# Kernel optimization log

Hardware: AMD Instinct MI355X
Metric: run time of the kernel (lower is better)

The kernel has to match this reference:

```python
import jax, jax.numpy as jnp
import numpy as np

B, N, D, OUT = 4, 4096, 2048, 2048
E, RANK, TOP_K = 8, 16, 2
ALPHA = 16.0
SCALING = ALPHA / RANK


def setup_inputs() -> dict:
    key = jax.random.key(0)
    k1, k2, k3, k4 = jax.random.split(key, 4)
    x = jax.random.normal(k1, (B, N, D), dtype=jnp.float32)
    weight = jax.random.normal(k2, (OUT, D), dtype=jnp.float32) * (1.0 / np.sqrt(D))
    router_w = jax.random.normal(k3, (E, D), dtype=jnp.float32) * 0.02
    experts_A = jax.random.normal(k4, (E, D, RANK), dtype=jnp.float32) * (1.0 / np.sqrt(RANK))
    # experts_B is zero-initialized in the module; use small random values so the
    # LoRA branch contributes non-trivially to the output for kernel testing.
    experts_B = jax.random.normal(jax.random.fold_in(key, 5), (E, RANK, OUT), dtype=jnp.float32) * 0.02
    return {"x": x, "weight": weight, "router_w": router_w,
            "experts_A": experts_A, "experts_B": experts_B}


def reference(x, weight, router_w, experts_A, experts_B):
    # base = F.linear(x, weight)  (no bias)
    base = jnp.einsum('bnd,od->bno', x, weight)
    # router logits: x @ W_r^T -> (B, N, E)
    logits = jnp.einsum('bnd,ed->bne', x, router_w)
    # top-k sparse routing: keep top-k logits, set rest to -inf, softmax
    topk_vals, topk_idx = jax.lax.top_k(logits, TOP_K)  # (B,N,K)
    keep = jax.nn.one_hot(topk_idx, E, dtype=jnp.bool_).any(axis=-2)  # (B,N,E)
    masked = jnp.where(keep, logits, -jnp.inf)
    router_weights = jax.nn.softmax(masked, axis=-1)  # (B,N,E)
    # per-expert low-rank down/up projection, weighted by router
    lora_down = jnp.einsum('bnd,edr->bner', x, experts_A)  # (B,N,E,rank)
    weighted = lora_down * router_weights[..., None]
    moe_out = jnp.einsum('bner,erd->bnd', weighted, experts_B)  # (B,N,OUT)
    return base + SCALING * moe_out
```

## Files before the change

kernel.cpp:

```cpp
#include <hip/hip_runtime.h>
#include <stdint.h>

#define D_DIM 2048
#define OUT_DIM 2048
#define NTOK 16384
#define SCALING 1.0f
#define NT32 68

typedef unsigned short u16;
typedef __attribute__((ext_vector_type(8))) short s16x8;
typedef __attribute__((ext_vector_type(4))) float f32x4;

#define WZ_OFF  0u
#define AZ_OFF  8388608u
#define BZ_OFF  8912896u
#define CZ_OFF  9437184u
#define W8_OFF  13631488u
#define XB_OFF  14155776u
#define WS_BIG   81264640u

__device__ inline u16 f2bf(float f) {
  union { float f; uint32_t u; } v; v.f = f;
  uint32_t u = v.u;
  u += 0x7FFFu + ((u >> 16) & 1u);
  return (u16)(u >> 16);
}

__device__ inline int swz32(int c, int row) {
  return (c & ~31) | (((((c >> 3) & 3) ^ ((row >> 1) & 3))) << 3) | (c & 7);
}

__global__ __launch_bounds__(256) void k_prep_router(
    const float* __restrict__ W, const float* __restrict__ A,
    const float* __restrict__ Bf, const float* __restrict__ x,
    const float* __restrict__ rw,
    u16* __restrict__ Wz, u16* __restrict__ Az, u16* __restrict__ Bz,
    float* __restrict__ w8, u16* __restrict__ xb) {
  int bid = blockIdx.x;
  if (bid < 4096) {
    int idx = bid * 256 + threadIdx.x;
    int o  = idx >> 9;
    int k0 = (idx & 511) * 4;
    const float4 v = *(const float4*)&W[(size_t)o * D_DIM + k0];
    int dst = swz32(k0, o);
    uint32_t p0 = (uint32_t)f2bf(v.x) | ((uint32_t)f2bf(v.y) << 16);
    uint32_t p1 = (uint32_t)f2bf(v.z) | ((uint32_t)f2bf(v.w) << 16);
    *(uint2*)&Wz[(size_t)o * D_DIM + dst] = make_uint2(p0, p1);
    return;
  }
  if (bid < 5120) {
    int idx = (bid - 4096) * 256 + threadIdx.x;
    float v = A[idx];
    int r = idx & 15;
    int d = (idx >> 4) & 2047;
    int e = idx >> 15;
    int er = e * 16 + r;
    Az[(size_t)er * D_DIM + swz32(d, er)] = f2bf(v);
    return;
  }
  if (bid < 6144) {
    int idx = (bid - 5120) * 256 + threadIdx.x;
    float v = Bf[idx];
    int er = idx >> 11;
    int o  = idx & 2047;
    Bz[(size_t)o * 128 + swz32(er, o)] = f2bf(v);
    return;
  }
  int lane = threadIdx.x & 63, wid = threadIdx.x >> 6;
  int t = (bid - 6144) * 4 + wid;
  const float* xr = x + (size_t)t * D_DIM;
  float4 xv[8];
#pragma unroll
  for (int j = 0; j < 8; ++j) xv[j] = *(const float4*)&xr[j * 256 + lane * 4];
#pragma unroll
  for (int j = 0; j < 8; ++j) {
    int c4 = j * 256 + lane * 4;
    int dst = swz32(c4, t);
    uint32_t p0 = (uint32_t)f2bf(xv[j].x) | ((uint32_t)f2bf(xv[j].y) << 16);
    uint32_t p1 = (uint32_t)f2bf(xv[j].z) | ((uint32_t)f2bf(xv[j].w) << 16);
    *(uint2*)&xb[(size_t)t * D_DIM + dst] = make_uint2(p0, p1);
  }
  float lg[8];
#pragma unroll
  for (int e = 0; e < 8; ++e) {
    float a = 0.f;
#pragma unroll
    for (int j = 0; j < 8; ++j) {
      float4 rv = *(const float4*)&rw[e * D_DIM + j * 256 + lane * 4];
      a = fmaf(xv[j].x, rv.x, a); a = fmaf(xv[j].y, rv.y, a);
      a = fmaf(xv[j].z, rv.z, a); a = fmaf(xv[j].w, rv.w, a);
    }
#pragma unroll
    for (int off = 32; off; off >>= 1) a += __shfl_xor(a, off, 64);
    lg[e] = a;
  }
  int i0 = 0;
#pragma unroll
  for (int e = 1; e < 8; ++e) if (lg[e] > lg[i0]) i0 = e;
  int i1 = (i0 == 0) ? 1 : 0;
#pragma unroll
  for (int e = 0; e < 8; ++e) if (e != i0 && lg[e] > lg[i1]) i1 = e;
  float e1 = expf(lg[i1] - lg[i0]);
  float inv = 1.f / (1.f + e1);
  float w0 = inv * SCALING, w1 = e1 * inv * SCALING;
  if (lane < 8)
    w8[(size_t)t * 8 + lane] = (lane == i0) ? w0 : (lane == i1) ? w1 : 0.f;
}

__global__ __launch_bounds__(256) void k_lora64(const u16* __restrict__ xb,
                                                const u16* __restrict__ Az,
                                                const float* __restrict__ w8,
                                                u16* __restrict__ Cz) {
  __shared__ u16 Al[2][2][64 * 32];
  __shared__ u16 Bl[2][2][128 * 32];
  __shared__ float w8s[64 * 8];
  int tid = threadIdx.x, lane = tid & 63, wid = tid >> 6;
  int t0 = blockIdx.x * 64;
  w8s[tid] = w8[(size_t)t0 * 8 + tid];
  w8s[256 + tid] = w8[(size_t)t0 * 8 + 256 + tid];
  f32x4 acc[8];
#pragma unroll
  for (int n = 0; n < 8; ++n) acc[n] = (f32x4){0.f, 0.f, 0.f, 0.f};
  const int l15 = lane & 15;
  const int gA = (lane >> 4) ^ ((l15 >> 1) & 3);
  const int arow = tid >> 2, c8 = (tid & 3) * 8;

  auto stage = [&](int kc, int buf) {
    if (kc > 31) kc = 31;
#pragma unroll
    for (int kk = 0; kk < 2; ++kk) {
      const u16* ga = xb + (size_t)(t0 + arow) * D_DIM + kc * 64 + kk * 32 + c8;
      __builtin_amdgcn_global_load_lds(
          (const __attribute__((address_space(1))) void*)ga,
          (__attribute__((address_space(3))) void*)(&Al[buf][kk][0] + tid * 8), 16, 0, 0);
#pragma unroll
      for (int i = 0; i < 2; ++i) {
        const u16* gb = Az + (size_t)(i * 64 + arow) * D_DIM + kc * 64 + kk * 32 + c8;
        __builtin_amdgcn_global_load_lds(
            (const __attribute__((address_space(1))) void*)gb,
            (__attribute__((address_space(3))) void*)(&Bl[buf][kk][0] + i * 2048 + tid * 8), 16, 0, 0);
      }
    }
  };

  stage(0, 0);
  asm volatile("s_waitcnt vmcnt(0)" ::: "memory");
  __builtin_amdgcn_s_barrier();
  const int aoff = (wid * 16 + l15) * 32 + gA * 8;
  for (int kc = 0; kc < 32; ++kc) {
    int cur = kc & 1;
    stage(kc + 1, cur ^ 1);
#pragma unroll
    for (int kk = 0; kk < 2; ++kk) {
      s16x8 af = *(const s16x8*)&Al[cur][kk][aoff];
#pragma unroll
      for (int nf = 0; nf < 8; ++nf) {
        s16x8 bf = *(const s16x8*)&Bl[cur][kk][(nf * 16 + l15) * 32 + gA * 8];
        acc[nf] = __builtin_amdgcn_mfma_f32_16x16x32_bf16(af, bf, acc[nf], 0, 0, 0);
      }
    }
    asm volatile("s_waitcnt vmcnt(0)" ::: "memory");
    __builtin_amdgcn_s_barrier();
  }
#pragma unroll
  for (int q = 0; q < 4; ++q) {
    int rloc = wid * 16 + (lane >> 4) * 4 + q;
#pragma unroll
    for (int nf = 0; nf < 8; ++nf) {
      int er = nf * 16 + l15;
      float v = acc[nf][q] * w8s[rloc * 8 + (er >> 4)];
      Cz[(size_t)(t0 + rloc) * 128 + swz32(er, rloc)] = f2bf(v);
    }
  }
}

__global__ __launch_bounds__(512, 2) void k_main32(const u16* __restrict__ xb,
                                                   const u16* __restrict__ Wz,
                                                   const u16* __restrict__ Cz,
                                                   const u16* __restrict__ Bz,
                                                   float* __restrict__ out) {
  __shared__ u16 AL[4][8192];
  __shared__ u16 BL[4][8192];
  const int tid = threadIdx.x, lane = tid & 63;
  const int wid = tid >> 6, wm = wid >> 2, wn = wid & 3;
  int bid = blockIdx.x;
  int swz = (bid & 7) * 64 + (bid >> 3);
  int mt = swz >> 3, nt = swz & 7;
  int t0 = mt * 256, o0 = nt * 256;
  const int l15 = lane & 15;
  const int gA = (lane >> 4) ^ ((l15 >> 1) & 3);
  const int aoff = (wm * 128 + l15) * 32 + gA * 8;
  const int boff = (wn * 64 + l15) * 32 + gA * 8;
  const int srow = tid >> 2, sc8 = (tid & 3) * 8;

  f32x4 acc[8][4];
#pragma unroll
  for (int m = 0; m < 8; ++m)
#pragma unroll
    for (int n = 0; n < 4; ++n) acc[m][n] = (f32x4){0.f, 0.f, 0.f, 0.f};
  s16x8 aA[8], bA[4], aB[8], bB[4];

  auto stg = [&](int t, int bufi) {
    if (t > NT32 - 1) t = NT32 - 1;
    const u16 *sa, *sb; int lda, ldb, ca;
    if (t < 64) { sa = xb; lda = D_DIM; sb = Wz; ldb = D_DIM; ca = t * 32; }
    else        { sa = Cz; lda = 128;   sb = Bz; ldb = 128;   ca = (t - 64) * 32; }
#pragma unroll
    for (int i = 0; i < 2; ++i) {
      const u16* g = sa + (size_t)(t0 + i * 128 + srow) * lda + ca + sc8;
      __builtin_amdgcn_global_load_lds(
          (const __attribute__((address_space(1))) void*)g,
          (__attribute__((address_space(3))) void*)(&AL[bufi][0] + i * 4096 + tid * 8), 16, 0, 0);
    }
#pragma unroll
    for (int i = 0; i < 2; ++i) {
      const u16* g = sb + (size_t)(o0 + i * 128 + srow) * ldb + ca + sc8;
      __builtin_amdgcn_global_load_lds(
          (const __attribute__((address_space(1))) void*)g,
          (__attribute__((address_space(3))) void*)(&BL[bufi][0] + i * 4096 + tid * 8), 16, 0, 0);
    }
  };

#define RD(av, bv, bufi) do {                                           \
    const u16* ap_ = &AL[bufi][aoff];                                   \
    const u16* bp_ = &BL[bufi][boff];                                   \
    _Pragma("unroll") for (int i_ = 0; i_ < 8; ++i_)                    \
      av[i_] = *(const s16x8*)(ap_ + i_ * 512);                         \
    _Pragma("unroll") for (int j_ = 0; j_ < 4; ++j_)                    \
      bv[j_] = *(const s16x8*)(bp_ + j_ * 512);                         \
  } while (0)

#define MM(av, bv) do {                                                 \
    _Pragma("unroll") for (int mf_ = 0; mf_ < 8; ++mf_)                 \
      _Pragma("unroll") for (int nf_ = 0; nf_ < 4; ++nf_)               \
        acc[mf_][nf_] = __builtin_amdgcn_mfma_f32_16x16x32_bf16(        \
            av[mf_], bv[nf_], acc[mf_][nf_], 0, 0, 0);                  \
  } while (0)

  stg(0, 0); stg(1, 1); stg(2, 2);
  asm volatile("s_waitcnt vmcnt(4)" ::: "memory");
  __builtin_amdgcn_s_barrier();
  RD(aA, bA, 0);

  for (int jj = 0; jj < NT32; jj += 2) {
    RD(aB, bB, (jj + 1) & 3);
    MM(aA, bA);
    stg(jj + 3, (jj + 3) & 3);
    asm volatile("s_waitcnt vmcnt(4)" ::: "memory");
    __builtin_amdgcn_s_barrier();
    RD(aA, bA, (jj + 2) & 3);
    MM(aB, bB);
    stg(jj + 4, (jj + 4) & 3);
    asm volatile("s_waitcnt vmcnt(4)" ::: "memory");
    __builtin_amdgcn_s_barrier();
  }
  asm volatile("s_waitcnt vmcnt(0) lgkmcnt(0)" ::: "memory");
#undef RD
#undef MM

#pragma unroll
  for (int mf = 0; mf < 8; ++mf)
#pragma unroll
    for (int q = 0; q < 4; ++q) {
      int row = t0 + wm * 128 + mf * 16 + (lane >> 4) * 4 + q;
#pragma unroll
      for (int nf = 0; nf < 4; ++nf) {
        int col = o0 + wn * 64 + nf * 16 + l15;
        out[(size_t)row * OUT_DIM + col] = acc[mf][nf][q];
      }
    }
}

extern "C" void kernel_launch(void* const* d_in, const int* in_sizes, int n_in,
                              void* d_out, int out_size, void* d_ws, size_t ws_size,
                              hipStream_t stream) {
  const float* x  = (const float*)d_in[0];
  const float* W  = (const float*)d_in[1];
  const float* rw = (const float*)d_in[2];
  const float* eA = (const float*)d_in[3];
  const float* eB = (const float*)d_in[4];
  float* out = (float*)d_out;
  char* ws = (char*)d_ws;
  if (ws_size < WS_BIG) return;

  u16*   Wz = (u16*)(ws + WZ_OFF);
  u16*   Az = (u16*)(ws + AZ_OFF);
  u16*   Bz = (u16*)(ws + BZ_OFF);
  u16*   Cz = (u16*)(ws + CZ_OFF);
  float* w8 = (float*)(ws + W8_OFF);
  u16*   xb = (u16*)(ws + XB_OFF);

  k_prep_router<<<10240, 256, 0, stream>>>(W, eA, eB, x, rw, Wz, Az, Bz, w8, xb);
  k_lora64<<<256, 256, 0, stream>>>(xb, Az, w8, Cz);
  k_main32<<<512, 512, 0, stream>>>(xb, Wz, Cz, Bz, out);
}
```

Baseline: 243.9 us.

## Fuse router and x conversion into LoRA kernel; shrink main GEMM tile to 128x128

Moves the x-to-bf16 conversion and router logit/top-2 softmax out of the prep kernel and into the LoRA down-projection kernel. That kernel reads fp32 x directly, writes both xb and its LDS tile, and accumulates router partial sums along the way, which removes the separate w8 buffer and one read of xb. The main GEMM changes from 256x256 tiles with 512 threads and a 4-stage buffer to 128x128 tiles with 256 threads and double buffering. This trades operand reuse for more blocks and occupancy. The fused LoRA kernel now runs only 256 blocks doing scalar conversion work, which could serialise x conversion on few CUs.

Measured after the change: 257.8 us. 1.06x slower.

```diff
diff --git a/kernel.cpp b/kernel.cpp
--- a/kernel.cpp
+++ b/kernel.cpp
@@ -15,7 +15,6 @@
 #define AZ_OFF  8388608u
 #define BZ_OFF  8912896u
 #define CZ_OFF  9437184u
-#define W8_OFF  13631488u
 #define XB_OFF  14155776u
 #define WS_BIG   81264640u
 
@@ -30,12 +29,16 @@
   return (c & ~31) | (((((c >> 3) & 3) ^ ((row >> 1) & 3))) << 3) | (c & 7);
 }
 
-__global__ __launch_bounds__(256) void k_prep_router(
-    const float* __restrict__ W, const float* __restrict__ A,
-    const float* __restrict__ Bf, const float* __restrict__ x,
-    const float* __restrict__ rw,
-    u16* __restrict__ Wz, u16* __restrict__ Az, u16* __restrict__ Bz,
-    float* __restrict__ w8, u16* __restrict__ xb) {
+#define GLDS(gp, lp) __builtin_amdgcn_global_load_lds( \
+    (const __attribute__((address_space(1))) void*)(gp), \
+    (__attribute__((address_space(3))) void*)(lp), 16, 0, 0)
+
+__global__ __launch_bounds__(256) void k_prep(const float* __restrict__ W,
+                                              const float* __restrict__ A,
+                                              const float* __restrict__ Bf,
+                                              u16* __restrict__ Wz,
+                                              u16* __restrict__ Az,
+                                              u16* __restrict__ Bz) {
   int bid = blockIdx.x;
   if (bid < 4096) {
     int idx = bid * 256 + threadIdx.x;
@@ -58,147 +61,155 @@
     Az[(size_t)er * D_DIM + swz32(d, er)] = f2bf(v);
     return;
   }
-  if (bid < 6144) {
+  {
     int idx = (bid - 5120) * 256 + threadIdx.x;
     float v = Bf[idx];
     int er = idx >> 11;
     int o  = idx & 2047;
     Bz[(size_t)o * 128 + swz32(er, o)] = f2bf(v);
-    return;
-  }
-  int lane = threadIdx.x & 63, wid = threadIdx.x >> 6;
-  int t = (bid - 6144) * 4 + wid;
-  const float* xr = x + (size_t)t * D_DIM;
-  float4 xv[8];
-#pragma unroll
-  for (int j = 0; j < 8; ++j) xv[j] = *(const float4*)&xr[j * 256 + lane * 4];
-#pragma unroll
-  for (int j = 0; j < 8; ++j) {
-    int c4 = j * 256 + lane * 4;
-    int dst = swz32(c4, t);
-    uint32_t p0 = (uint32_t)f2bf(xv[j].x) | ((uint32_t)f2bf(xv[j].y) << 16);
-    uint32_t p1 = (uint32_t)f2bf(xv[j].z) | ((uint32_t)f2bf(xv[j].w) << 16);
-    *(uint2*)&xb[(size_t)t * D_DIM + dst] = make_uint2(p0, p1);
-  }
-  float lg[8];
-#pragma unroll
-  for (int e = 0; e < 8; ++e) {
-    float a = 0.f;
-#pragma unroll
-    for (int j = 0; j < 8; ++j) {
-      float4 rv = *(const float4*)&rw[e * D_DIM + j * 256 + lane * 4];
-      a = fmaf(xv[j].x, rv.x, a); a = fmaf(xv[j].y, rv.y, a);
-      a = fmaf(xv[j].z, rv.z, a); a = fmaf(xv[j].w, rv.w, a);
-    }
-#pragma unroll
-    for (int off = 32; off; off >>= 1) a += __shfl_xor(a, off, 64);
-    lg[e] = a;
-  }
-  int i0 = 0;
-#pragma unroll
-  for (int e = 1; e < 8; ++e) if (lg[e] > lg[i0]) i0 = e;
-  int i1 = (i0 == 0) ? 1 : 0;
-#pragma unroll
-  for (int e = 0; e < 8; ++e) if (e != i0 && lg[e] > lg[i1]) i1 = e;
-  float e1 = expf(lg[i1] - lg[i0]);
-  float inv = 1.f / (1.f + e1);
-  float w0 = inv * SCALING, w1 = e1 * inv * SCALING;
-  if (lane < 8)
-    w8[(size_t)t * 8 + lane] = (lane == i0) ? w0 : (lane == i1) ? w1 : 0.f;
-}
-
-__global__ __launch_bounds__(256) void k_lora64(const u16* __restrict__ xb,
-                                                const u16* __restrict__ Az,
-                                                const float* __restrict__ w8,
-                                                u16* __restrict__ Cz) {
-  __shared__ u16 Al[2][2][64 * 32];
-  __shared__ u16 Bl[2][2][128 * 32];
+  }
+}
+
+__global__ __launch_bounds__(256) void k_router_lora(
+    const float* __restrict__ x, const float* __restrict__ rw,
+    const u16* __restrict__ Az, u16* __restrict__ xb, u16* __restrict__ Cz) {
+  __shared__ u16 Axl[2][64 * 64];
+  __shared__ u16 Bzl[2][128 * 64];
   __shared__ float w8s[64 * 8];
   int tid = threadIdx.x, lane = tid & 63, wid = tid >> 6;
   int t0 = blockIdx.x * 64;
-  w8s[tid] = w8[(size_t)t0 * 8 + tid];
-  w8s[256 + tid] = w8[(size_t)t0 * 8 + 256 + tid];
+  const int l15 = lane & 15;
+
   f32x4 acc[8];
 #pragma unroll
   for (int n = 0; n < 8; ++n) acc[n] = (f32x4){0.f, 0.f, 0.f, 0.f};
-  const int l15 = lane & 15;
-  const int gA = (lane >> 4) ^ ((l15 >> 1) & 3);
-  const int arow = tid >> 2, c8 = (tid & 3) * 8;
+  float lgp[4][8];
+#pragma unroll
+  for (int i = 0; i < 4; ++i)
+#pragma unroll
+    for (int e = 0; e < 8; ++e) lgp[i][e] = 0.f;
 
   auto stage = [&](int kc, int buf) {
-    if (kc > 31) kc = 31;
-#pragma unroll
-    for (int kk = 0; kk < 2; ++kk) {
-      const u16* ga = xb + (size_t)(t0 + arow) * D_DIM + kc * 64 + kk * 32 + c8;
-      __builtin_amdgcn_global_load_lds(
-          (const __attribute__((address_space(1))) void*)ga,
-          (__attribute__((address_space(3))) void*)(&Al[buf][kk][0] + tid * 8), 16, 0, 0);
-#pragma unroll
-      for (int i = 0; i < 2; ++i) {
-        const u16* gb = Az + (size_t)(i * 64 + arow) * D_DIM + kc * 64 + kk * 32 + c8;
-        __builtin_amdgcn_global_load_lds(
-            (const __attribute__((address_space(1))) void*)gb,
-            (__attribute__((address_space(3))) void*)(&Bl[buf][kk][0] + i * 2048 + tid * 8), 16, 0, 0);
+    bool real = (kc <= 31);
+    if (!real) kc = 31;
+    const int c4 = (tid & 15) * 4;
+    float4 rv[8];
+    if (real) {
+#pragma unroll
+      for (int e = 0; e < 8; ++e)
+        rv[e] = *(const float4*)&rw[(size_t)e * D_DIM + kc * 64 + c4];
+    }
+#pragma unroll
+    for (int i = 0; i < 4; ++i) {
+      int row = i * 16 + (tid >> 4);
+      float4 v = *(const float4*)&x[(size_t)(t0 + row) * D_DIM + kc * 64 + c4];
+      uint32_t p0 = (uint32_t)f2bf(v.x) | ((uint32_t)f2bf(v.y) << 16);
+      uint32_t p1 = (uint32_t)f2bf(v.z) | ((uint32_t)f2bf(v.w) << 16);
+      *(uint2*)&xb[(size_t)(t0 + row) * D_DIM + swz32(kc * 64 + c4, row)] =
+          make_uint2(p0, p1);
+      *(uint2*)&Axl[buf][row * 64 + swz32(c4, row)] = make_uint2(p0, p1);
+      if (real) {
+#pragma unroll
+        for (int e = 0; e < 8; ++e) {
+          lgp[i][e] = fmaf(v.x, rv[e].x, lgp[i][e]);
+          lgp[i][e] = fmaf(v.y, rv[e].y, lgp[i][e]);
+          lgp[i][e] = fmaf(v.z, rv[e].z, lgp[i][e]);
+          lgp[i][e] = fmaf(v.w, rv[e].w, lgp[i][e]);
+        }
       }
     }
+#pragma unroll
+    for (int i = 0; i < 4; ++i) {
+      const u16* g = Az + (size_t)(i * 32 + (tid >> 3)) * D_DIM + kc * 64 + (tid & 7) * 8;
+      GLDS(g, &Bzl[buf][0] + i * 2048 + tid * 8);
+    }
   };
 
   stage(0, 0);
-  asm volatile("s_waitcnt vmcnt(0)" ::: "memory");
+  asm volatile("s_waitcnt vmcnt(0) lgkmcnt(0)" ::: "memory");
   __builtin_amdgcn_s_barrier();
-  const int aoff = (wid * 16 + l15) * 32 + gA * 8;
+
   for (int kc = 0; kc < 32; ++kc) {
     int cur = kc & 1;
     stage(kc + 1, cur ^ 1);
+    const int g = (lane >> 4) ^ ((l15 >> 1) & 3);
 #pragma unroll
     for (int kk = 0; kk < 2; ++kk) {
-      s16x8 af = *(const s16x8*)&Al[cur][kk][aoff];
+      s16x8 af = *(const s16x8*)&Axl[cur][(wid * 16 + l15) * 64 + kk * 32 + g * 8];
 #pragma unroll
       for (int nf = 0; nf < 8; ++nf) {
-        s16x8 bf = *(const s16x8*)&Bl[cur][kk][(nf * 16 + l15) * 32 + gA * 8];
+        s16x8 bf = *(const s16x8*)&Bzl[cur][(nf * 16 + l15) * 64 + kk * 32 + g * 8];
         acc[nf] = __builtin_amdgcn_mfma_f32_16x16x32_bf16(af, bf, acc[nf], 0, 0, 0);
       }
     }
-    asm volatile("s_waitcnt vmcnt(0)" ::: "memory");
+    asm volatile("s_waitcnt vmcnt(0) lgkmcnt(0)" ::: "memory");
     __builtin_amdgcn_s_barrier();
   }
+
+#pragma unroll
+  for (int i = 0; i < 4; ++i) {
+#pragma unroll
+    for (int e = 0; e < 8; ++e) {
+      float v = lgp[i][e];
+      v += __shfl_xor(v, 1, 64);
+      v += __shfl_xor(v, 2, 64);
+      v += __shfl_xor(v, 4, 64);
+      v += __shfl_xor(v, 8, 64);
+      lgp[i][e] = v;
+    }
+    float l0 = lgp[i][0]; int i0 = 0;
+#pragma unroll
+    for (int e = 1; e < 8; ++e) if (lgp[i][e] > l0) { l0 = lgp[i][e]; i0 = e; }
+    float l1 = -3e38f; int i1 = 0;
+#pragma unroll
+    for (int e = 0; e < 8; ++e) if (e != i0 && lgp[i][e] > l1) { l1 = lgp[i][e]; i1 = e; }
+    float e1 = expf(l1 - l0);
+    float inv = 1.f / (1.f + e1);
+    if (l15 < 8) {
+      int row = i * 16 + (tid >> 4);
+      w8s[row * 8 + l15] =
+          (l15 == i0) ? inv * SCALING : (l15 == i1) ? e1 * inv * SCALING : 0.f;
+    }
+  }
+  __syncthreads();
+
 #pragma unroll
   for (int q = 0; q < 4; ++q) {
-    int rloc = wid * 16 + (lane >> 4) * 4 + q;
+    int rl = wid * 16 + (lane >> 4) * 4 + q;
 #pragma unroll
     for (int nf = 0; nf < 8; ++nf) {
+      float v = acc[nf][q] * w8s[rl * 8 + nf];
       int er = nf * 16 + l15;
-      float v = acc[nf][q] * w8s[rloc * 8 + (er >> 4)];
-      Cz[(size_t)(t0 + rloc) * 128 + swz32(er, rloc)] = f2bf(v);
-    }
-  }
-}
-
-__global__ __launch_bounds__(512, 2) void k_main32(const u16* __restrict__ xb,
-                                                   const u16* __restrict__ Wz,
-                                                   const u16* __restrict__ Cz,
-                                                   const u16* __restrict__ Bz,
-                                                   float* __restrict__ out) {
-  __shared__ u16 AL[4][8192];
-  __shared__ u16 BL[4][8192];
+      Cz[(size_t)(t0 + rl) * 128 + swz32(er, rl)] = f2bf(v);
+    }
+  }
+}
+
+__global__ __launch_bounds__(256, 3) void k_main128(const u16* __restrict__ xb,
+                                                    const u16* __restrict__ Wz,
+                                                    const u16* __restrict__ Cz,
+                                                    const u16* __restrict__ Bz,
+                                                    float* __restrict__ out) {
+  __shared__ u16 AL[2][4096];
+  __shared__ u16 BL[2][4096];
   const int tid = threadIdx.x, lane = tid & 63;
-  const int wid = tid >> 6, wm = wid >> 2, wn = wid & 3;
+  const int wid = tid >> 6, wm = wid >> 1, wn = wid & 1;
   int bid = blockIdx.x;
-  int swz = (bid & 7) * 64 + (bid >> 3);
-  int mt = swz >> 3, nt = swz & 7;
-  int t0 = mt * 256, o0 = nt * 256;
+  int swz = (bid & 7) * 256 + (bid >> 3);
+  int mt = swz >> 4, nt = swz & 15;
+  int t0 = mt * 128, o0 = nt * 128;
   const int l15 = lane & 15;
   const int gA = (lane >> 4) ^ ((l15 >> 1) & 3);
-  const int aoff = (wm * 128 + l15) * 32 + gA * 8;
+  const int aoff = (wm * 64 + l15) * 32 + gA * 8;
   const int boff = (wn * 64 + l15) * 32 + gA * 8;
   const int srow = tid >> 2, sc8 = (tid & 3) * 8;
 
-  f32x4 acc[8][4];
-#pragma unroll
-  for (int m = 0; m < 8; ++m)
+  f32x4 acc[4][4];
+#pragma unroll
+  for (int m = 0; m < 4; ++m)
 #pragma unroll
     for (int n = 0; n < 4; ++n) acc[m][n] = (f32x4){0.f, 0.f, 0.f, 0.f};
-  s16x8 aA[8], bA[4], aB[8], bB[4];
+  s16x8 aA[4], bA[4], aB[4], bB[4];
 
   auto stg = [&](int t, int bufi) {
     if (t > NT32 - 1) t = NT32 - 1;
@@ -207,62 +218,55 @@
     else        { sa = Cz; lda = 128;   sb = Bz; ldb = 128;   ca = (t - 64) * 32; }
 #pragma unroll
     for (int i = 0; i < 2; ++i) {
-      const u16* g = sa + (size_t)(t0 + i * 128 + srow) * lda + ca + sc8;
-      __builtin_amdgcn_global_load_lds(
-          (const __attribute__((address_space(1))) void*)g,
-          (__attribute__((address_space(3))) void*)(&AL[bufi][0] + i * 4096 + tid * 8), 16, 0, 0);
-    }
-#pragma unroll
-    for (int i = 0; i < 2; ++i) {
-      const u16* g = sb + (size_t)(o0 + i * 128 + srow) * ldb + ca + sc8;
-      __builtin_amdgcn_global_load_lds(
-          (const __attribute__((address_space(1))) void*)g,
-          (__attribute__((address_space(3))) void*)(&BL[bufi][0] + i * 4096 + tid * 8), 16, 0, 0);
+      const u16* g = sa + (size_t)(t0 + i * 64 + srow) * lda + ca + sc8;
+      GLDS(g, &AL[bufi][0] + i * 2048 + tid * 8);
+      const u16* h = sb + (size_t)(o0 + i * 64 + srow) * ldb + ca + sc8;
+      GLDS(h, &BL[bufi][0] + i * 2048 + tid * 8);
     }
   };
 
-#define RD(av, bv, bufi) do {                                           \
-    const u16* ap_ = &AL[bufi][aoff];                                   \
-    const u16* bp_ = &BL[bufi][boff];                                   \
-    _Pragma("unroll") for (int i_ = 0; i_ < 8; ++i_)                    \
-      av[i_] = *(const s16x8*)(ap_ + i_ * 512);                         \
-    _Pragma("unroll") for (int j_ = 0; j_ < 4; ++j_)                    \
-      bv[j_] = *(const s16x8*)(bp_ + j_ * 512);                         \
+#define RD(av, bv, bufi) do {                                            \
+    _Pragma("unroll") for (int i_ = 0; i_ < 4; ++i_)                     \
+      av[i_] = *(const s16x8*)&AL[bufi][aoff + i_ * 512];                \
+    _Pragma("unroll") for (int j_ = 0; j_ < 4; ++j_)                     \
+      bv[j_] = *(const s16x8*)&BL[bufi][boff + j_ * 512];                \
   } while (0)
 
-#define MM(av, bv) do {                                                 \
-    _Pragma("unroll") for (int mf_ = 0; mf_ < 8; ++mf_)                 \
-      _Pragma("unroll") for (int nf_ = 0; nf_ < 4; ++nf_)               \
-        acc[mf_][nf_] = __builtin_amdgcn_mfma_f32_16x16x32_bf16(        \
-            av[mf_], bv[nf_], acc[mf_][nf_], 0, 0, 0);                  \
+#define MM(av, bv) do {                                                  \
+    _Pragma("unroll") for (int mf_ = 0; mf_ < 4; ++mf_)                  \
+      _Pragma("unroll") for (int nf_ = 0; nf_ < 4; ++nf_)                \
+        acc[mf_][nf_] = __builtin_amdgcn_mfma_f32_16x16x32_bf16(         \
+            av[mf_], bv[nf_], acc[mf_][nf_], 0, 0, 0);                   \
   } while (0)
 
-  stg(0, 0); stg(1, 1); stg(2, 2);
-  asm volatile("s_waitcnt vmcnt(4)" ::: "memory");
+  stg(0, 0);
+  asm volatile("s_waitcnt vmcnt(0)" ::: "memory");
   __builtin_amdgcn_s_barrier();
   RD(aA, bA, 0);
+  stg(1, 1);
+  asm volatile("s_waitcnt vmcnt(0) lgkmcnt(0)" ::: "memory");
+  __builtin_amdgcn_s_barrier();
 
   for (int jj = 0; jj < NT32; jj += 2) {
-    RD(aB, bB, (jj + 1) & 3);
+    RD(aB, bB, 1);
+    stg(jj + 2, 0);
     MM(aA, bA);
-    stg(jj + 3, (jj + 3) & 3);
-    asm volatile("s_waitcnt vmcnt(4)" ::: "memory");
+    asm volatile("s_waitcnt vmcnt(0) lgkmcnt(0)" ::: "memory");
     __builtin_amdgcn_s_barrier();
-    RD(aA, bA, (jj + 2) & 3);
+    RD(aA, bA, 0);
+    stg(jj + 3, 1);
     MM(aB, bB);
-    stg(jj + 4, (jj + 4) & 3);
-    asm volatile("s_waitcnt vmcnt(4)" ::: "memory");
+    asm volatile("s_waitcnt vmcnt(0) lgkmcnt(0)" ::: "memory");
     __builtin_amdgcn_s_barrier();
   }
-  asm volatile("s_waitcnt vmcnt(0) lgkmcnt(0)" ::: "memory");
 #undef RD
 #undef MM
 
 #pragma unroll
-  for (int mf = 0; mf < 8; ++mf)
+  for (int mf = 0; mf < 4; ++mf)
 #pragma unroll
     for (int q = 0; q < 4; ++q) {
-      int row = t0 + wm * 128 + mf * 16 + (lane >> 4) * 4 + q;
+      int row = t0 + wm * 64 + mf * 16 + (lane >> 4) * 4 + q;
 #pragma unroll
       for (int nf = 0; nf < 4; ++nf) {
         int col = o0 + wn * 64 + nf * 16 + l15;
@@ -283,14 +287,13 @@
   char* ws = (char*)d_ws;
   if (ws_size < WS_BIG) return;
 
-  u16*   Wz = (u16*)(ws + WZ_OFF);
-  u16*   Az = (u16*)(ws + AZ_OFF);
-  u16*   Bz = (u16*)(ws + BZ_OFF);
-  u16*   Cz = (u16*)(ws + CZ_OFF);
-  float* w8 = (float*)(ws + W8_OFF);
-  u16*   xb = (u16*)(ws + XB_OFF);
-
-  k_prep_router<<<10240, 256, 0, stream>>>(W, eA, eB, x, rw, Wz, Az, Bz, w8, xb);
-  k_lora64<<<256, 256, 0, stream>>>(xb, Az, w8, Cz);
-  k_main32<<<512, 512, 0, stream>>>(xb, Wz, Cz, Bz, out);
-}
+  u16* Wz = (u16*)(ws + WZ_OFF);
+  u16* Az = (u16*)(ws + AZ_OFF);
+  u16* Bz = (u16*)(ws + BZ_OFF);
+  u16* Cz = (u16*)(ws + CZ_OFF);
+  u16* xb = (u16*)(ws + XB_OFF);
+
+  k_prep<<<6144, 256, 0, stream>>>(W, eA, eB, Wz, Az, Bz);
+  k_router_lora<<<256, 256, 0, stream>>>(x, rw, Az, xb, Cz);
+  k_main128<<<2048, 256, 0, stream>>>(xb, Wz, Cz, Bz, out);
+}
```
